# Performance work log

Measured on AMD Instinct MI355X. Metric: run time of the kernel, lower is better.

## Reference

```python
import jax, jax.numpy as jnp
import numpy as np

# --- MLA config (matches init_kwargs) ---
DIM = 2048
H = 16
KV_RANK = 512
Q_RANK = 1536
ROPE = 64          # qk_rope_head_dim (even)
NOPE = 128         # qk_nope_head_dim
VD = 128           # v_head_dim
THETA = 500000.0
EPS = 1e-6
B, T = 1, 2048
QK_HEAD = NOPE + ROPE  # logits use nope + rope dims


def _rmsnorm(x, w):
    # x float32; RMS over last dim, no mean subtraction
    rms = jax.lax.rsqrt(jnp.mean(x * x, axis=-1, keepdims=True) + EPS)
    return (x * rms) * w


def _rope_tables(t):
    inv_freq = 1.0 / (THETA ** (jnp.arange(0, ROPE, 2, dtype=jnp.float32) / ROPE))  # (ROPE/2,)
    pos = jnp.arange(t, dtype=jnp.float32)
    angles = jnp.outer(pos, inv_freq)  # (T, ROPE/2)
    return jnp.cos(angles), jnp.sin(angles)


def _apply_rope(x, cos, sin):
    # x: (B, T, Hx, D) with adjacent-pair rotation; cos/sin: (T, D/2)
    b, t, h, d = x.shape
    xp = x.reshape(b, t, h, d // 2, 2)
    even, odd = xp[..., 0], xp[..., 1]
    c = cos.reshape(1, t, 1, d // 2)
    s = sin.reshape(1, t, 1, d // 2)
    out = jnp.stack((even * c - odd * s, odd * c + even * s), axis=-1)
    return out.reshape(b, t, h, d)


def setup_inputs() -> dict:
    key = jax.random.key(0)
    ks = jax.random.split(key, 7)
    s = 0.02
    x = jax.random.normal(ks[0], (B, T, DIM), dtype=jnp.float32)
    w_q_down = jax.random.normal(ks[1], (Q_RANK, DIM), dtype=jnp.float32) * s
    q_norm_w = jnp.ones((Q_RANK,), dtype=jnp.float32)
    w_q_up = jax.random.normal(ks[2], (H * (NOPE + ROPE), Q_RANK), dtype=jnp.float32) * s
    w_kv_down = jax.random.normal(ks[3], (KV_RANK + ROPE, DIM), dtype=jnp.float32) * s
    kv_norm_w = jnp.ones((KV_RANK,), dtype=jnp.float32)
    w_kv_up = jax.random.normal(ks[4], (H * (NOPE + VD), KV_RANK), dtype=jnp.float32) * s
    w_o = jax.random.normal(ks[5], (DIM, H * VD), dtype=jnp.float32) * s
    return {"x": x, "w_q_down": w_q_down, "q_norm_w": q_norm_w, "w_q_up": w_q_up,
            "w_kv_down": w_kv_down, "kv_norm_w": kv_norm_w, "w_kv_up": w_kv_up, "w_o": w_o}


def reference(x, w_q_down, q_norm_w, w_q_up, w_kv_down, kv_norm_w, w_kv_up, w_o):
    b, t, _ = x.shape
    # Query path: down-proj -> RMSNorm -> up-proj, split nope/rope
    c_q = _rmsnorm(x @ w_q_down.T, q_norm_w)                       # (B,T,Q_RANK)
    q = (c_q @ w_q_up.T).reshape(b, t, H, NOPE + ROPE)
    q_nope, q_rope = q[..., :NOPE], q[..., NOPE:]
    # KV path: down-proj -> split latent c_kv and shared rope key
    kv = x @ w_kv_down.T                                           # (B,T,KV_RANK+ROPE)
    c_kv = kv[..., :KV_RANK]
    k_rope_raw = kv[..., KV_RANK:].reshape(b, t, 1, ROPE)
    # RoPE (adjacent-pair), start_pos=0
    cos, sin = _rope_tables(t)
    q_rope = _apply_rope(q_rope, cos, sin)
    k_rope = _apply_rope(k_rope_raw, cos, sin)                     # (B,T,1,ROPE) shared head
    # Reconstruct k_nope and v from normalized latent
    kv_up = (_rmsnorm(c_kv, kv_norm_w) @ w_kv_up.T).reshape(b, t, H, NOPE + VD)
    k_nope, v = kv_up[..., :NOPE], kv_up[..., NOPE:]
    # Assemble full q/k (rope key broadcast across heads)
    q_full = jnp.concatenate((q_nope, q_rope), axis=-1)            # (B,T,H,QK_HEAD)
    k_full = jnp.concatenate((k_nope, jnp.broadcast_to(k_rope, (b, t, H, ROPE))), axis=-1)
    # Causal attention
    scale = 1.0 / np.sqrt(QK_HEAD)
    scores = jnp.einsum('bqhd,bkhd->bhqk', q_full, k_full) * scale  # (B,H,T,T)
    causal = jnp.tril(jnp.ones((t, t), dtype=bool))
    scores = jnp.where(causal[None, None], scores, -jnp.inf)
    attn = jax.nn.softmax(scores, axis=-1)
    out = jnp.einsum('bhqk,bkhd->bqhd', attn, v).reshape(b, t, H * VD)
    return out @ w_o.T                                             # (B,T,DIM)
```

## Files before the change

### kernel.cpp

```cpp
#include <hip/hip_runtime.h>
#include <hip/hip_bf16.h>

typedef short short8 __attribute__((ext_vector_type(8)));
typedef float f32x4 __attribute__((ext_vector_type(4)));

#define DIM 2048
#define NH 16
#define KV_RANK 512
#define Q_RANK 1536
#define ROPE_D 64
#define NOPE 128
#define VD 128
#define TT 2048
#define QKH 192
#define QD (NH * QKH)
#define KVUP_D (NH * (NOPE + VD))
#define WDN 2176

__device__ inline unsigned short f2bf(float f) {
  __hip_bfloat16 h = __float2bfloat16(f);
  union { __hip_bfloat16 h; unsigned short u; } cv; cv.h = h; return cv.u;
}
__device__ inline float bf2f(unsigned short u) {
  union { unsigned int i; float f; } cv; cv.i = ((unsigned int)u) << 16; return cv.f;
}
__device__ inline void gload_lds16(const void* g, void* l) {
  __builtin_amdgcn_global_load_lds(
      (const __attribute__((address_space(1))) void*)g,
      (__attribute__((address_space(3))) void*)l, 16, 0, 0);
}

__global__ __launch_bounds__(256) void convert_all(
    const float* __restrict__ x, const float* __restrict__ wqd,
    const float* __restrict__ wkvd, const float* __restrict__ wqu,
    const float* __restrict__ wkvu, const float* __restrict__ wo,
    unsigned short* __restrict__ xb, unsigned short* __restrict__ wdb,
    unsigned short* __restrict__ wqub, unsigned short* __restrict__ wkvub,
    unsigned short* __restrict__ wob) {
  int i = blockIdx.x * 256 + threadIdx.x;
  const int n0 = TT * DIM / 4;
  const int n1 = WDN * 2048 / 4;
  const int n2 = QD * Q_RANK / 4;
  const int n3 = KVUP_D * KV_RANK / 4;
  const int n4 = DIM * DIM / 4;
  float4 v;
  unsigned short* dst;
  if (i < n0) { v = reinterpret_cast<const float4*>(x)[i]; dst = xb; }
  else if ((i -= n0) < n1) {
    int row = i >> 9, c4 = i & 511;
    if (row < 1536)      v = reinterpret_cast<const float4*>(wqd)[row * 512 + c4];
    else if (row < 2112) v = reinterpret_cast<const float4*>(wkvd)[(row - 1536) * 512 + c4];
    else                 v = make_float4(0.f, 0.f, 0.f, 0.f);
    dst = wdb;
  }
  else if ((i -= n1) < n2) { v = reinterpret_cast<const float4*>(wqu)[i]; dst = wqub; }
  else if ((i -= n2) < n3) { v = reinterpret_cast<const float4*>(wkvu)[i]; dst = wkvub; }
  else if ((i -= n3) < n4) { v = reinterpret_cast<const float4*>(wo)[i]; dst = wob; }
  else return;
  ushort4 o;
  o.x = f2bf(v.x); o.y = f2bf(v.y); o.z = f2bf(v.z); o.w = f2bf(v.w);
  reinterpret_cast<ushort4*>(dst)[i] = o;
}

__device__ __forceinline__ void gemm_core(const unsigned short* __restrict__ A,
                                          const unsigned short* __restrict__ W,
                                          unsigned short* As, unsigned short* Bs,
                                          int K, int lda, int ldb,
                                          int bm, int bn, int tid,
                                          f32x4 (&acc)[4][4]) {
  const int lane = tid & 63, wave = tid >> 6;
  const int wm = (wave >> 1) * 64, wn = (wave & 1) * 64;
  const int fr = lane & 15, fg = lane >> 4;
  const int sr = lane >> 3, scb = (lane & 7) ^ sr;
  const int r0 = wave * 32;

  const unsigned short* Ag = A + (size_t)(bm + r0 + sr) * lda + scb * 8;
  const unsigned short* Wg = W + (size_t)(bn + r0 + sr) * ldb + scb * 8;
  const int nt = K >> 6;

#pragma unroll
  for (int i = 0; i < 4; ++i) {
    gload_lds16(Ag + (size_t)(i * 8) * lda, As + r0 * 64 + i * 512);
    gload_lds16(Wg + (size_t)(i * 8) * ldb, Bs + r0 * 64 + i * 512);
  }
  int cur = 0;
  for (int t = 0; t < nt; ++t) {
    if (t + 1 < nt) {
      const int nb = cur ^ 1;
      const int ko = (t + 1) * 64;
#pragma unroll
      for (int i = 0; i < 4; ++i) {
        gload_lds16(Ag + ko + (size_t)(i * 8) * lda, As + nb * 8192 + r0 * 64 + i * 512);
        gload_lds16(Wg + ko + (size_t)(i * 8) * ldb, Bs + nb * 8192 + r0 * 64 + i * 512);
      }
      asm volatile("s_waitcnt vmcnt(8)" ::: "memory");
    } else {
      asm volatile("s_waitcnt vmcnt(0)" ::: "memory");
    }
    __builtin_amdgcn_s_barrier();
    asm volatile("" ::: "memory");
    const unsigned short* Ac = As + cur * 8192;
    const unsigned short* Bc = Bs + cur * 8192;
    __builtin_amdgcn_s_setprio(1);
#pragma unroll
    for (int kk = 0; kk < 2; ++kk) {
      short8 a[4], b[4];
#pragma unroll
      for (int i = 0; i < 4; ++i) {
        int ra = wm + i * 16 + fr;
        a[i] = *reinterpret_cast<const short8*>(&Ac[ra * 64 + (((kk * 4 + fg) ^ (ra & 7)) * 8)]);
        int rb = wn + i * 16 + fr;
        b[i] = *reinterpret_cast<const short8*>(&Bc[rb * 64 + (((kk * 4 + fg) ^ (rb & 7)) * 8)]);
      }
#pragma unroll
      for (int i = 0; i < 4; ++i)
#pragma unroll
        for (int j = 0; j < 4; ++j)
          acc[i][j] = __builtin_amdgcn_mfma_f32_16x16x32_bf16(a[i], b[j], acc[i][j], 0, 0, 0);
    }
    __builtin_amdgcn_s_setprio(0);
    asm volatile("" ::: "memory");
    __builtin_amdgcn_s_barrier();
    cur ^= 1;
  }
}

__global__ __launch_bounds__(256) void gemm_fast(const unsigned short* __restrict__ A,
                                                 const unsigned short* __restrict__ W,
                                                 float* __restrict__ Cf,
                                                 unsigned short* __restrict__ Cb,
                                                 int K, int lda, int ldb, int ldc) {
  __shared__ __align__(16) unsigned short As[2 * 128 * 64];
  __shared__ __align__(16) unsigned short Bs[2 * 128 * 64];
  const int tid = threadIdx.x;
  const int bm = blockIdx.y * 128, bn = blockIdx.x * 128;
  const int lane = tid & 63, wave = tid >> 6;
  const int wm = (wave >> 1) * 64, wn = (wave & 1) * 64;
  const int fr = lane & 15, fg = lane >> 4;

  f32x4 acc[4][4] = {};
  gemm_core(A, W, As, Bs, K, lda, ldb, bm, bn, tid, acc);

  if (Cb) {
#pragma unroll
    for (int i = 0; i < 4; ++i) {
      int row0 = bm + wm + i * 16 + fg * 4;
#pragma unroll
      for (int j = 0; j < 4; ++j) {
        int col = bn + wn + j * 16 + fr;
#pragma unroll
        for (int r = 0; r < 4; ++r)
          Cb[(size_t)(row0 + r) * ldc + col] = f2bf(acc[i][j][r]);
      }
    }
  } else {
#pragma unroll
    for (int i = 0; i < 4; ++i) {
      int row0 = bm + wm + i * 16 + fg * 4;
#pragma unroll
      for (int j = 0; j < 4; ++j) {
        int col = bn + wn + j * 16 + fr;
#pragma unroll
        for (int r = 0; r < 4; ++r)
          Cf[(size_t)(row0 + r) * ldc + col] = acc[i][j][r];
      }
    }
  }
}

__global__ __launch_bounds__(256) void gemm_dual(
    const unsigned short* __restrict__ A1, const unsigned short* __restrict__ W1,
    unsigned short* __restrict__ C1,
    const unsigned short* __restrict__ A2, const unsigned short* __restrict__ W2,
    unsigned short* __restrict__ kbuf, unsigned short* __restrict__ vt) {
  __shared__ __align__(16) unsigned short As[2 * 128 * 64];
  __shared__ __align__(16) unsigned short Bs[2 * 128 * 64];
  const int tid = threadIdx.x;
  const int bx = blockIdx.x;
  const unsigned short *A, *W;
  int K, lda, bm, bn;
  const bool isq = (bx < 384);
  if (isq) {
    A = A1; W = W1; K = Q_RANK; lda = Q_RANK;
    bn = (bx % 24) * 128; bm = (bx / 24) * 128;
  } else {
    int b2 = bx - 384;
    A = A2; W = W2; K = KV_RANK; lda = KV_RANK;
    bn = (b2 & 31) * 128; bm = (b2 >> 5) * 128;
  }
  const int lane = tid & 63, wave = tid >> 6;
  const int wm = (wave >> 1) * 64, wn = (wave & 1) * 64;
  const int fr = lane & 15, fg = lane >> 4;

  f32x4 acc[4][4] = {};
  gemm_core(A, W, As, Bs, K, lda, lda, bm, bn, tid, acc);

  if (isq) {
#pragma unroll
    for (int i = 0; i < 4; ++i) {
      int row0 = bm + wm + i * 16 + fg * 4;
#pragma unroll
      for (int j = 0; j < 4; ++j) {
        int col = bn + wn + j * 16 + fr;
#pragma unroll
        for (int r = 0; r < 4; ++r)
          C1[(size_t)(row0 + r) * QD + col] = f2bf(acc[i][j][r]);
      }
    }
  } else {
#pragma unroll
    for (int i = 0; i < 4; ++i) {
      int row0 = bm + wm + i * 16 + fg * 4;
#pragma unroll
      for (int j = 0; j < 4; ++j) {
        int col = bn + wn + j * 16 + fr;
        int hh = col >> 8, cc = col & 255;
        if (cc < 128) {
#pragma unroll
          for (int r = 0; r < 4; ++r)
            kbuf[((size_t)hh * TT + row0 + r) * QKH + cc] = f2bf(acc[i][j][r]);
        } else {
          ushort4 w4;
          w4.x = f2bf(acc[i][j][0]); w4.y = f2bf(acc[i][j][1]);
          w4.z = f2bf(acc[i][j][2]); w4.w = f2bf(acc[i][j][3]);
          *reinterpret_cast<ushort4*>(vt + (size_t)(hh * VD + cc - 128) * TT + row0) = w4;
        }
      }
    }
  }
}

__global__ __launch_bounds__(256) void rmsnorm_bf16(const unsigned short* __restrict__ in,
                                                    int instride, int inoff,
                                                    const float* __restrict__ w,
                                                    unsigned short* __restrict__ out,
                                                    int outstride, int cols) {
  const int row = blockIdx.x, tid = threadIdx.x;
  const unsigned short* x = in + (size_t)row * instride + inoff;
  const int nch = cols >> 3;
  float ss = 0.f;
  for (int cb = tid; cb < nch; cb += 256) {
    short8 v = *reinterpret_cast<const short8*>(x + cb * 8);
#pragma unroll
    for (int e = 0; e < 8; ++e) { float f = bf2f((unsigned short)v[e]); ss += f * f; }
  }
  __shared__ float red[256];
  red[tid] = ss; __syncthreads();
  for (int off = 128; off > 0; off >>= 1) {
    if (tid < off) red[tid] += red[tid + off];
    __syncthreads();
  }
  float r = rsqrtf(red[0] / (float)cols + 1e-6f);
  for (int cb = tid; cb < nch; cb += 256) {
    short8 v = *reinterpret_cast<const short8*>(x + cb * 8);
    ushort4 o0, o1;
    o0.x = f2bf(bf2f((unsigned short)v[0]) * r * w[cb * 8 + 0]);
    o0.y = f2bf(bf2f((unsigned short)v[1]) * r * w[cb * 8 + 1]);
    o0.z = f2bf(bf2f((unsigned short)v[2]) * r * w[cb * 8 + 2]);
    o0.w = f2bf(bf2f((unsigned short)v[3]) * r * w[cb * 8 + 3]);
    o1.x = f2bf(bf2f((unsigned short)v[4]) * r * w[cb * 8 + 4]);
    o1.y = f2bf(bf2f((unsigned short)v[5]) * r * w[cb * 8 + 5]);
    o1.z = f2bf(bf2f((unsigned short)v[6]) * r * w[cb * 8 + 6]);
    o1.w = f2bf(bf2f((unsigned short)v[7]) * r * w[cb * 8 + 7]);
    *reinterpret_cast<ushort4*>(out + (size_t)row * outstride + cb * 8) = o0;
    *reinterpret_cast<ushort4*>(out + (size_t)row * outstride + cb * 8 + 4) = o1;
  }
}

__global__ __launch_bounds__(256) void rope_kernel(unsigned short* __restrict__ qb,
                                                   const unsigned short* __restrict__ cqkv,
                                                   unsigned short* __restrict__ kbuf) {
  const int t = blockIdx.x, tid = threadIdx.x;
  unsigned short* qrow = qb + (size_t)t * QD;
  for (int p = tid; p < NH * 32 + 32; p += 256) {
    int j = (p < NH * 32) ? (p & 31) : (p - NH * 32);
    float inv = powf(500000.0f, -(float)(2 * j) * (1.0f / 64.0f));
    float ang = (float)t * inv;
    float sv, cv;
    sincosf(ang, &sv, &cv);
    if (p < NH * 32) {
      int h = p >> 5;
      unsigned short* b = qrow + h * QKH + NOPE + 2 * j;
      float e = bf2f(b[0]), o = bf2f(b[1]);
      b[0] = f2bf(e * cv - o * sv);
      b[1] = f2bf(o * cv + e * sv);
    } else {
      const unsigned short* b = cqkv + (size_t)t * WDN + 2048 + 2 * j;
      float e = bf2f(b[0]), o = bf2f(b[1]);
      unsigned short re = f2bf(e * cv - o * sv);
      unsigned short ro = f2bf(o * cv + e * sv);
#pragma unroll
      for (int hh = 0; hh < NH; ++hh) {
        kbuf[((size_t)hh * TT + t) * QKH + NOPE + 2 * j]     = re;
        kbuf[((size_t)hh * TT + t) * QKH + NOPE + 2 * j + 1] = ro;
      }
    }
  }
}

__global__ __launch_bounds__(256, 2) void attn_part(
    const unsigned short* __restrict__ qb,
    const unsigned short* __restrict__ kbuf,
    const unsigned short* __restrict__ vtb,
    unsigned short* __restrict__ Opart,
    float* __restrict__ ml)
{
  const int b = blockIdx.x;
  const int h = b & 15;
  const int w = b >> 4;
  int qt, c;
  if (w < 16)      { qt = 15 - (w >> 2); c = w & 3; }
  else if (w < 28) { int v = w - 16; qt = 11 - v / 3; c = v % 3; }
  else if (w < 36) { int v = w - 28; qt = 7 - ((w - 28) >> 1); c = v & 1; }
  else             { qt = 3 - (w - 36); c = 0; }
  const int t0 = qt * 128;
  const int ktlo = c * 8;
  const int kthi = min(c * 8 + 8, 2 * qt + 2);
  const int tid = threadIdx.x;
  const int lane = tid & 63, wv = tid >> 6;
  const int fr = lane & 15, fg = lane >> 4;

  __shared__ __align__(16) unsigned short KVl[2560 * 8];
  __shared__ __align__(16) unsigned short Ps[4][16 * 64];
  unsigned short* Kl = KVl;
  unsigned short* Vt = KVl + 12288;

  short8 qf[2][6];
#pragma unroll
  for (int s = 0; s < 2; ++s) {
    const unsigned short* qrow = qb + (size_t)(t0 + wv * 32 + s * 16 + fr) * QD + h * QKH;
#pragma unroll
    for (int kc = 0; kc < 6; ++kc)
      qf[s][kc] = *reinterpret_cast<const short8*>(qrow + kc * 32 + fg * 8);
  }

  f32x4 o[2][8] = {};
  float m2[2] = {-1e30f, -1e30f};
  float l2[2] = {0.f, 0.f};
  const float scale = 0.0721687836487032f;
  const unsigned short* kb = kbuf + (size_t)h * TT * QKH;
  const unsigned short* vb = vtb + (size_t)h * VD * TT;

  for (int kt = ktlo; kt < kthi; ++kt) {
    const int kt0 = kt * 64;
#pragma unroll
    for (int i = 0; i < 6; ++i) {
      int u = tid + i * 256;
      int row = u / 24, cb = u - (u / 24) * 24;
      int cbs = cb ^ (row & 7);
      gload_lds16(kb + (size_t)(kt0 + row) * QKH + cbs * 8, Kl + u * 8);
    }
#pragma unroll
    for (int i = 0; i < 4; ++i) {
      int u = tid + i * 256;
      int d = u >> 3, cb = u & 7;
      int cbs = cb ^ (d & 7);
      gload_lds16(vb + (size_t)d * TT + kt0 + cbs * 8, Vt + u * 8);
    }
    asm volatile("s_waitcnt vmcnt(0)" ::: "memory");
    __syncthreads();

    f32x4 sA[2][4] = {};
    __builtin_amdgcn_s_setprio(1);
#pragma unroll
    for (int kc = 0; kc < 6; ++kc) {
#pragma unroll
      for (int kr = 0; kr < 4; ++kr) {
        int row = kr * 16 + fr;
        short8 kf = *reinterpret_cast<const short8*>(
            &Kl[row * QKH + (((kc * 4 + fg) ^ (row & 7)) * 8)]);
        sA[0][kr] = __builtin_amdgcn_mfma_f32_16x16x32_bf16(kf, qf[0][kc], sA[0][kr], 0, 0, 0);
        sA[1][kr] = __builtin_amdgcn_mfma_f32_16x16x32_bf16(kf, qf[1][kc], sA[1][kr], 0, 0, 0);
      }
    }
    __builtin_amdgcn_s_setprio(0);

    const bool diag = (kt0 + 64 > t0);
#pragma unroll
    for (int s = 0; s < 2; ++s) {
      const int qg = t0 + wv * 32 + s * 16 + fr;
      float mx = -1e30f;
#pragma unroll
      for (int kr = 0; kr < 4; ++kr)
#pragma unroll
        for (int r = 0; r < 4; ++r) {
          float svv = sA[s][kr][r] * scale;
          if (diag && (kt0 + kr * 16 + fg * 4 + r) > qg) svv = -1e30f;
          sA[s][kr][r] = svv;
          mx = fmaxf(mx, svv);
        }
      mx = fmaxf(mx, __shfl_xor(mx, 16));
      mx = fmaxf(mx, __shfl_xor(mx, 32));
      float mn = fmaxf(m2[s], mx);
      float corr = __expf(m2[s] - mn);
      m2[s] = mn;
      float ssum = 0.f;
#pragma unroll
      for (int kr = 0; kr < 4; ++kr) {
        ushort4 pk;
        float p0 = __expf(sA[s][kr][0] - mn);
        float p1 = __expf(sA[s][kr][1] - mn);
        float p2 = __expf(sA[s][kr][2] - mn);
        float p3 = __expf(sA[s][kr][3] - mn);
        ssum += p0 + p1 + p2 + p3;
        pk.x = f2bf(p0); pk.y = f2bf(p1); pk.z = f2bf(p2); pk.w = f2bf(p3);
        *reinterpret_cast<ushort4*>(
            &Ps[wv][fr * 64 + (((kr * 2 + (fg >> 1)) ^ (fr & 7)) * 8) + (fg & 1) * 4]) = pk;
      }
      ssum += __shfl_xor(ssum, 16);
      ssum += __shfl_xor(ssum, 32);
      l2[s] = l2[s] * corr + ssum;
      if (__any(corr != 1.0f)) {
        float c0 = __shfl(corr, fg * 4 + 0);
        float c1 = __shfl(corr, fg * 4 + 1);
        float c2 = __shfl(corr, fg * 4 + 2);
        float c3 = __shfl(corr, fg * 4 + 3);
#pragma unroll
        for (int dj = 0; dj < 8; ++dj) {
          o[s][dj][0] *= c0; o[s][dj][1] *= c1;
          o[s][dj][2] *= c2; o[s][dj][3] *= c3;
        }
      }
      __builtin_amdgcn_s_setprio(1);
#pragma unroll
      for (int kk = 0; kk < 2; ++kk) {
        short8 pa = *reinterpret_cast<const short8*>(
            &Ps[wv][fr * 64 + (((kk * 4 + fg) ^ (fr & 7)) * 8)]);
#pragma unroll
        for (int dj = 0; dj < 8; ++dj) {
          int dv = dj * 16 + fr;
          short8 bv = *reinterpret_cast<const short8*>(
              &Vt[dv * 64 + (((kk * 4 + fg) ^ (dv & 7)) * 8)]);
          o[s][dj] = __builtin_amdgcn_mfma_f32_16x16x32_bf16(pa, bv, o[s][dj], 0, 0, 0);
        }
      }
      __builtin_amdgcn_s_setprio(0);
    }
    __syncthreads();
  }

  const int slot = (h * 16 + qt) * 4 + c;
#pragma unroll
  for (int s = 0; s < 2; ++s) {
#pragma unroll
    for (int r = 0; r < 4; ++r) {
      int row = wv * 32 + s * 16 + fg * 4 + r;
      unsigned short* orow = Opart + ((size_t)slot * 128 + row) * 128;
#pragma unroll
      for (int dj = 0; dj < 8; ++dj)
        orow[dj * 16 + fr] = f2bf(o[s][dj][r]);
    }
    if (fg == 0) {
      int row = wv * 32 + s * 16 + fr;
      ml[((size_t)slot * 128 + row) * 2]     = m2[s];
      ml[((size_t)slot * 128 + row) * 2 + 1] = l2[s];
    }
  }
}

__global__ __launch_bounds__(256) void attn_combine(
    const unsigned short* __restrict__ Opart, const float* __restrict__ ml,
    unsigned short* __restrict__ out) {
  const int bid = blockIdx.x;
  const int h = bid >> 5;
  const int qt = (bid >> 1) & 15;
  const int rh = bid & 1;
  const int nch = qt / 4 + 1;
  const int tid = threadIdx.x;
  const int row = rh * 64 + (tid >> 2), dg = tid & 3;
  const int base = (h * 16 + qt) * 4;
  float mm[4], ll[4];
  float M = -1e30f;
#pragma unroll
  for (int cc = 0; cc < 4; ++cc) {
    if (cc < nch) {
      mm[cc] = ml[((size_t)(base + cc) * 128 + row) * 2];
      ll[cc] = ml[((size_t)(base + cc) * 128 + row) * 2 + 1];
      M = fmaxf(M, mm[cc]);
    } else { mm[cc] = -1e30f; ll[cc] = 0.f; }
  }
  float L = 0.f;
#pragma unroll
  for (int cc = 0; cc < 4; ++cc) {
    mm[cc] = __expf(mm[cc] - M);
    L += ll[cc] * mm[cc];
  }
  float acc[32] = {};
#pragma unroll
  for (int cc = 0; cc < 4; ++cc) {
    if (cc < nch) {
      const unsigned short* op = Opart + ((size_t)(base + cc) * 128 + row) * 128 + dg * 32;
      float sc = mm[cc];
#pragma unroll
      for (int e8 = 0; e8 < 4; ++e8) {
        short8 v = *reinterpret_cast<const short8*>(op + e8 * 8);
#pragma unroll
        for (int e = 0; e < 8; ++e) acc[e8 * 8 + e] += bf2f((unsigned short)v[e]) * sc;
      }
    }
  }
  float linv = 1.0f / L;
  unsigned short* dst = out + (size_t)(qt * 128 + row) * DIM + h * VD + dg * 32;
#pragma unroll
  for (int e4 = 0; e4 < 8; ++e4) {
    ushort4 w4;
    w4.x = f2bf(acc[e4 * 4 + 0] * linv);
    w4.y = f2bf(acc[e4 * 4 + 1] * linv);
    w4.z = f2bf(acc[e4 * 4 + 2] * linv);
    w4.w = f2bf(acc[e4 * 4 + 3] * linv);
    *reinterpret_cast<ushort4*>(dst + e4 * 4) = w4;
  }
}

extern "C" void kernel_launch(void* const* d_in, const int* in_sizes, int n_in,
                              void* d_out, int out_size, void* d_ws, size_t ws_size,
                              hipStream_t stream) {
  const float* x        = (const float*)d_in[0];
  const float* w_q_down = (const float*)d_in[1];
  const float* q_norm_w = (const float*)d_in[2];
  const float* w_q_up   = (const float*)d_in[3];
  const float* w_kv_down= (const float*)d_in[4];
  const float* kv_norm_w= (const float*)d_in[5];
  const float* w_kv_up  = (const float*)d_in[6];
  const float* w_o      = (const float*)d_in[7];
  float* outp = (float*)d_out;

  char* ws = (char*)d_ws;
  size_t off = 0;
  auto alloc = [&](size_t bytes) {
    void* p = ws + off;
    off += (bytes + 255) & ~(size_t)255;
    return p;
  };
  unsigned short* x_bf     = (unsigned short*)alloc((size_t)TT * DIM * 2);
  unsigned short* wdown_bf = (unsigned short*)alloc((size_t)WDN * DIM * 2);
  unsigned short* wqu_bf   = (unsigned short*)alloc((size_t)QD * Q_RANK * 2);
  unsigned short* wkvu_bf  = (unsigned short*)alloc((size_t)KVUP_D * KV_RANK * 2);
  unsigned short* wo_bf    = (unsigned short*)alloc((size_t)DIM * DIM * 2);
  unsigned short* cqkv_bf  = (unsigned short*)alloc((size_t)TT * WDN * 2);
  unsigned short* cq_bf    = (unsigned short*)alloc((size_t)TT * Q_RANK * 2);
  unsigned short* ckv_bf   = (unsigned short*)alloc((size_t)TT * KV_RANK * 2);
  unsigned short* qb_bf    = (unsigned short*)alloc((size_t)TT * QD * 2);
  unsigned short* kbuf     = (unsigned short*)alloc((size_t)NH * TT * QKH * 2);
  unsigned short* vtb      = (unsigned short*)alloc((size_t)NH * VD * TT * 2);
  unsigned short* Opart    = (unsigned short*)alloc((size_t)1024 * 128 * 128 * 2);
  float*          mlbuf    = (float*)alloc((size_t)1024 * 128 * 2 * 4);
  unsigned short* attn_bf  = x_bf;

  {
    int total = TT * DIM / 4 + WDN * 2048 / 4 + QD * Q_RANK / 4 +
                KVUP_D * KV_RANK / 4 + DIM * DIM / 4;
    convert_all<<<dim3((total + 255) / 256), dim3(256), 0, stream>>>(
        x, w_q_down, w_kv_down, w_q_up, w_kv_up, w_o,
        x_bf, wdown_bf, wqu_bf, wkvu_bf, wo_bf);
  }

  dim3 blk(256);
  gemm_fast<<<dim3(WDN / 128, TT / 128), blk, 0, stream>>>(
      x_bf, wdown_bf, nullptr, cqkv_bf, DIM, DIM, DIM, WDN);
  rmsnorm_bf16<<<dim3(TT), blk, 0, stream>>>(cqkv_bf, WDN, 0, q_norm_w, cq_bf, Q_RANK, Q_RANK);
  rmsnorm_bf16<<<dim3(TT), blk, 0, stream>>>(cqkv_bf, WDN, Q_RANK, kv_norm_w, ckv_bf, KV_RANK, KV_RANK);
  gemm_dual<<<dim3(896), blk, 0, stream>>>(cq_bf, wqu_bf, qb_bf,
                                           ckv_bf, wkvu_bf, kbuf, vtb);
  rope_kernel<<<dim3(TT), blk, 0, stream>>>(qb_bf, cqkv_bf, kbuf);
  attn_part<<<dim3(640), blk, 0, stream>>>(qb_bf, kbuf, vtb, Opart, mlbuf);
  attn_combine<<<dim3(512), blk, 0, stream>>>(Opart, mlbuf, attn_bf);
  gemm_fast<<<dim3(DIM / 128, TT / 128), blk, 0, stream>>>(
      attn_bf, wo_bf, outp, nullptr, DIM, DIM, DIM, DIM);
}
```

Before: 217.9 us.

## Swizzle GEMM workgroup order, fuse the two RMSNorms, batch PV MFMAs across subtiles

GEMM kernels remap linear workgroup IDs with an XCD-style stride-8 swizzle, so tiles dispatched to the same chiplet share operands in its L2. The two RMSNorm launches merge into one kernel that handles both the q and kv segments of each row, saving a launch and an extra pass over the row. In attention, P is now stored per subtile in a doubled LDS buffer, and the PV MFMAs for both 16-row subtiles run after both softmaxes, reusing each V fragment load twice. This costs more LDS for Ps and may raise register pressure at 2 blocks per CU.

```diff
diff --git a/kernel.cpp b/kernel.cpp
--- a/kernel.cpp
+++ b/kernel.cpp
@@ -133,7 +133,11 @@
   __shared__ __align__(16) unsigned short As[2 * 128 * 64];
   __shared__ __align__(16) unsigned short Bs[2 * 128 * 64];
   const int tid = threadIdx.x;
-  const int bm = blockIdx.y * 128, bn = blockIdx.x * 128;
+  const int w = blockIdx.y * gridDim.x + blockIdx.x;
+  const int nwg = gridDim.x * gridDim.y;
+  const int s = (w & 7) * (nwg >> 3) + (w >> 3);
+  const int bxs = s % gridDim.x, bys = s / gridDim.x;
+  const int bm = bys * 128, bn = bxs * 128;
   const int lane = tid & 63, wave = tid >> 6;
   const int wm = (wave >> 1) * 64, wn = (wave & 1) * 64;
   const int fr = lane & 15, fg = lane >> 4;
@@ -176,15 +180,17 @@
   __shared__ __align__(16) unsigned short As[2 * 128 * 64];
   __shared__ __align__(16) unsigned short Bs[2 * 128 * 64];
   const int tid = threadIdx.x;
-  const int bx = blockIdx.x;
+  const int w = blockIdx.x;
+  const int nwg = gridDim.x;
+  const int s = (w & 7) * (nwg >> 3) + (w >> 3);
   const unsigned short *A, *W;
   int K, lda, bm, bn;
-  const bool isq = (bx < 384);
+  const bool isq = (s < 384);
   if (isq) {
     A = A1; W = W1; K = Q_RANK; lda = Q_RANK;
-    bn = (bx % 24) * 128; bm = (bx / 24) * 128;
+    bn = (s % 24) * 128; bm = (s / 24) * 128;
   } else {
-    int b2 = bx - 384;
+    int b2 = s - 384;
     A = A2; W = W2; K = KV_RANK; lda = KV_RANK;
     bn = (b2 & 31) * 128; bm = (b2 >> 5) * 128;
   }
@@ -230,40 +236,48 @@
   }
 }
 
-__global__ __launch_bounds__(256) void rmsnorm_bf16(const unsigned short* __restrict__ in,
-                                                    int instride, int inoff,
-                                                    const float* __restrict__ w,
-                                                    unsigned short* __restrict__ out,
-                                                    int outstride, int cols) {
+__global__ __launch_bounds__(256) void rmsnorm_both(
+    const unsigned short* __restrict__ cqkv,
+    const float* __restrict__ qw, const float* __restrict__ kvw,
+    unsigned short* __restrict__ cq, unsigned short* __restrict__ ckv) {
   const int row = blockIdx.x, tid = threadIdx.x;
-  const unsigned short* x = in + (size_t)row * instride + inoff;
-  const int nch = cols >> 3;
-  float ss = 0.f;
-  for (int cb = tid; cb < nch; cb += 256) {
-    short8 v = *reinterpret_cast<const short8*>(x + cb * 8);
-#pragma unroll
-    for (int e = 0; e < 8; ++e) { float f = bf2f((unsigned short)v[e]); ss += f * f; }
-  }
   __shared__ float red[256];
-  red[tid] = ss; __syncthreads();
-  for (int off = 128; off > 0; off >>= 1) {
-    if (tid < off) red[tid] += red[tid + off];
+  const unsigned short* base = cqkv + (size_t)row * WDN;
+
+#pragma unroll
+  for (int ph = 0; ph < 2; ++ph) {
+    const int cols = ph ? KV_RANK : Q_RANK;
+    const int nch = cols >> 3;
+    const unsigned short* x = base + (ph ? Q_RANK : 0);
+    const float* w = ph ? kvw : qw;
+    unsigned short* out = (ph ? ckv : cq) + (size_t)row * cols;
+    float ss = 0.f;
+    for (int cb = tid; cb < nch; cb += 256) {
+      short8 v = *reinterpret_cast<const short8*>(x + cb * 8);
+#pragma unroll
+      for (int e = 0; e < 8; ++e) { float f = bf2f((unsigned short)v[e]); ss += f * f; }
+    }
+    red[tid] = ss; __syncthreads();
+    for (int off = 128; off > 0; off >>= 1) {
+      if (tid < off) red[tid] += red[tid + off];
+      __syncthreads();
+    }
+    float r = rsqrtf(red[0] / (float)cols + 1e-6f);
     __syncthreads();
-  }
-  float r = rsqrtf(red[0] / (float)cols + 1e-6f);
-  for (int cb = tid; cb < nch; cb += 256) {
-    short8 v = *reinterpret_cast<const short8*>(x + cb * 8);
-    ushort4 o0, o1;
-    o0.x = f2bf(bf2f((unsigned short)v[0]) * r * w[cb * 8 + 0]);
-    o0.y = f2bf(bf2f((unsigned short)v[1]) * r * w[cb * 8 + 1]);
-    o0.z = f2bf(bf2f((unsigned short)v[2]) * r * w[cb * 8 + 2]);
-    o0.w = f2bf(bf2f((unsigned short)v[3]) * r * w[cb * 8 + 3]);
-    o1.x = f2bf(bf2f((unsigned short)v[4]) * r * w[cb * 8 + 4]);
-    o1.y = f2bf(bf2f((unsigned short)v[5]) * r * w[cb * 8 + 5]);
-    o1.z = f2bf(bf2f((unsigned short)v[6]) * r * w[cb * 8 + 6]);
-    o1.w = f2bf(bf2f((unsigned short)v[7]) * r * w[cb * 8 + 7]);
-    *reinterpret_cast<ushort4*>(out + (size_t)row * outstride + cb * 8) = o0;
-    *reinterpret_cast<ushort4*>(out + (size_t)row * outstride + cb * 8 + 4) = o1;
+    for (int cb = tid; cb < nch; cb += 256) {
+      short8 v = *reinterpret_cast<const short8*>(x + cb * 8);
+      ushort4 o0, o1;
+      o0.x = f2bf(bf2f((unsigned short)v[0]) * r * w[cb * 8 + 0]);
+      o0.y = f2bf(bf2f((unsigned short)v[1]) * r * w[cb * 8 + 1]);
+      o0.z = f2bf(bf2f((unsigned short)v[2]) * r * w[cb * 8 + 2]);
+      o0.w = f2bf(bf2f((unsigned short)v[3]) * r * w[cb * 8 + 3]);
+      o1.x = f2bf(bf2f((unsigned short)v[4]) * r * w[cb * 8 + 4]);
+      o1.y = f2bf(bf2f((unsigned short)v[5]) * r * w[cb * 8 + 5]);
+      o1.z = f2bf(bf2f((unsigned short)v[6]) * r * w[cb * 8 + 6]);
+      o1.w = f2bf(bf2f((unsigned short)v[7]) * r * w[cb * 8 + 7]);
+      *reinterpret_cast<ushort4*>(out + cb * 8) = o0;
+      *reinterpret_cast<ushort4*>(out + cb * 8 + 4) = o1;
+    }
   }
 }
 
@@ -311,7 +325,7 @@
   int qt, c;
   if (w < 16)      { qt = 15 - (w >> 2); c = w & 3; }
   else if (w < 28) { int v = w - 16; qt = 11 - v / 3; c = v % 3; }
-  else if (w < 36) { int v = w - 28; qt = 7 - ((w - 28) >> 1); c = v & 1; }
+  else if (w < 36) { qt = 7 - ((w - 28) >> 1); c = (w - 28) & 1; }
   else             { qt = 3 - (w - 36); c = 0; }
   const int t0 = qt * 128;
   const int ktlo = c * 8;
@@ -321,7 +335,7 @@
   const int fr = lane & 15, fg = lane >> 4;
 
   __shared__ __align__(16) unsigned short KVl[2560 * 8];
-  __shared__ __align__(16) unsigned short Ps[4][16 * 64];
+  __shared__ __align__(16) unsigned short Ps[4][2][16 * 64];
   unsigned short* Kl = KVl;
   unsigned short* Vt = KVl + 12288;
 
@@ -405,7 +419,7 @@
         ssum += p0 + p1 + p2 + p3;
         pk.x = f2bf(p0); pk.y = f2bf(p1); pk.z = f2bf(p2); pk.w = f2bf(p3);
         *reinterpret_cast<ushort4*>(
-            &Ps[wv][fr * 64 + (((kr * 2 + (fg >> 1)) ^ (fr & 7)) * 8) + (fg & 1) * 4]) = pk;
+            &Ps[wv][s][fr * 64 + (((kr * 2 + (fg >> 1)) ^ (fr & 7)) * 8) + (fg & 1) * 4]) = pk;
       }
       ssum += __shfl_xor(ssum, 16);
       ssum += __shfl_xor(ssum, 32);
@@ -421,21 +435,25 @@
           o[s][dj][2] *= c2; o[s][dj][3] *= c3;
         }
       }
-      __builtin_amdgcn_s_setprio(1);
-#pragma unroll
-      for (int kk = 0; kk < 2; ++kk) {
-        short8 pa = *reinterpret_cast<const short8*>(
-            &Ps[wv][fr * 64 + (((kk * 4 + fg) ^ (fr & 7)) * 8)]);
-#pragma unroll
-        for (int dj = 0; dj < 8; ++dj) {
-          int dv = dj * 16 + fr;
-          short8 bv = *reinterpret_cast<const short8*>(
-              &Vt[dv * 64 + (((kk * 4 + fg) ^ (dv & 7)) * 8)]);
-          o[s][dj] = __builtin_amdgcn_mfma_f32_16x16x32_bf16(pa, bv, o[s][dj], 0, 0, 0);
-        }
-      }
-      __builtin_amdgcn_s_setprio(0);
-    }
+    }
+
+    __builtin_amdgcn_s_setprio(1);
+#pragma unroll
+    for (int kk = 0; kk < 2; ++kk) {
+      short8 pa0 = *reinterpret_cast<const short8*>(
+          &Ps[wv][0][fr * 64 + (((kk * 4 + fg) ^ (fr & 7)) * 8)]);
+      short8 pa1 = *reinterpret_cast<const short8*>(
+          &Ps[wv][1][fr * 64 + (((kk * 4 + fg) ^ (fr & 7)) * 8)]);
+#pragma unroll
+      for (int dj = 0; dj < 8; ++dj) {
+        int dv = dj * 16 + fr;
+        short8 bv = *reinterpret_cast<const short8*>(
+            &Vt[dv * 64 + (((kk * 4 + fg) ^ (dv & 7)) * 8)]);
+        o[0][dj] = __builtin_amdgcn_mfma_f32_16x16x32_bf16(pa0, bv, o[0][dj], 0, 0, 0);
+        o[1][dj] = __builtin_amdgcn_mfma_f32_16x16x32_bf16(pa1, bv, o[1][dj], 0, 0, 0);
+      }
+    }
+    __builtin_amdgcn_s_setprio(0);
     __syncthreads();
   }
 
@@ -558,8 +576,7 @@
   dim3 blk(256);
   gemm_fast<<<dim3(WDN / 128, TT / 128), blk, 0, stream>>>(
       x_bf, wdown_bf, nullptr, cqkv_bf, DIM, DIM, DIM, WDN);
-  rmsnorm_bf16<<<dim3(TT), blk, 0, stream>>>(cqkv_bf, WDN, 0, q_norm_w, cq_bf, Q_RANK, Q_RANK);
-  rmsnorm_bf16<<<dim3(TT), blk, 0, stream>>>(cqkv_bf, WDN, Q_RANK, kv_norm_w, ckv_bf, KV_RANK, KV_RANK);
+  rmsnorm_both<<<dim3(TT), blk, 0, stream>>>(cqkv_bf, q_norm_w, kv_norm_w, cq_bf, ckv_bf);
   gemm_dual<<<dim3(896), blk, 0, stream>>>(cq_bf, wqu_bf, qb_bf,
                                            ckv_bf, wkvu_bf, kbuf, vtb);
   rope_kernel<<<dim3(TT), blk, 0, stream>>>(qb_bf, cqkv_bf, kbuf);
```

Result: slower. 229.2 us (+5.2%).
